# Kernel optimization log

Measured on AMD Instinct MI355X. Metric: run time of the kernel, lower is better.

Reference implementation:

```python
import jax, jax.numpy as jnp
import numpy as np

SCALE = 0.02  # init scale for weight matrices


def setup_inputs() -> dict:
    B, M, H = 2048, 64, 1024
    key = jax.random.key(0)
    ks = jax.random.split(key, 10)
    inp = {
        "pose_embed": jax.random.normal(ks[0], (B, H), jnp.float32),
        "query_embed": jax.random.normal(ks[1], (B, H), jnp.float32),
        "h": jax.random.normal(ks[2], (B, H), jnp.float32),
        "c": jax.random.normal(ks[3], (B, H), jnp.float32),
        "memory": jax.random.normal(ks[4], (B, M, H), jnp.float32),
        "W_ih": jax.random.normal(ks[5], (4 * H, H), jnp.float32) * SCALE,
        "W_hh": jax.random.normal(ks[6], (4 * H, H), jnp.float32) * SCALE,
        "b_ih": jnp.zeros((4 * H,), jnp.float32),
        "b_hh": jnp.zeros((4 * H,), jnp.float32),
        "Wq": jax.random.normal(ks[7], (H, H), jnp.float32) * SCALE,
        "bq": jnp.zeros((H,), jnp.float32),
        "Wk": jax.random.normal(ks[8], (H, H), jnp.float32) * SCALE,
        "bk": jnp.zeros((H,), jnp.float32),
        "Wv": jax.random.normal(ks[9], (H, H), jnp.float32) * SCALE,
        "bv": jnp.zeros((H,), jnp.float32),
    }
    return inp


def reference(pose_embed, query_embed, h, c, memory,
              W_ih, W_hh, b_ih, b_hh, Wq, bq, Wk, bk, Wv, bv):
    H = pose_embed.shape[-1]
    # --- LSTMCell step (torch gate order: i, f, g, o) ---
    gates = pose_embed @ W_ih.T + b_ih + h @ W_hh.T + b_hh  # [B, 4H]
    i_g, f_g, g_g, o_g = jnp.split(gates, 4, axis=-1)
    c_new = jax.nn.sigmoid(f_g) * c + jax.nn.sigmoid(i_g) * jnp.tanh(g_g)
    h_new = jax.nn.sigmoid(o_g) * jnp.tanh(c_new)
    # --- FIFO memory update (detach, pop oldest, append new h) ---
    mem = jnp.concatenate(
        [memory[:, 1:], jax.lax.stop_gradient(h_new)[:, None]], axis=1)  # [B, M, H]
    # --- single-query attention over memory ---
    Q = query_embed @ Wq.T + bq                       # [B, H]
    K = mem @ Wk.T + bk                               # [B, M, H]
    V = mem @ Wv.T + bv                               # [B, M, H]
    scores = jnp.einsum('bh,bmh->bm', Q, K) / jnp.sqrt(jnp.float32(H))
    attn = jax.nn.softmax(scores, axis=-1)            # [B, M]
    attended = jnp.einsum('bm,bmh->bh', attn, V)      # [B, H]
    return attended, h_new, c_new
```

## Files before the change

### kernel.cpp

```cpp
#include <hip/hip_runtime.h>
#include <stdint.h>

typedef __attribute__((ext_vector_type(8))) short short8;
typedef __attribute__((ext_vector_type(4))) float f32x4;
typedef unsigned short u16;

__device__ __forceinline__ u16 f2bf(float f) {
  union { float f; uint32_t u; } v; v.f = f;
  return (u16)((v.u + 0x7FFFu + ((v.u >> 16) & 1u)) >> 16);
}

__device__ __forceinline__ void gl_lds16(const void* g, void* l) {
  __builtin_amdgcn_global_load_lds(
      (const __attribute__((address_space(1))) void*)g,
      (__attribute__((address_space(3))) void*)l, 16, 0, 0);
}

__global__ __launch_bounds__(256) void gemm_bt(
    const u16* __restrict__ A, const u16* __restrict__ B,
    float* __restrict__ Cf, u16* __restrict__ Cb,
    const float* __restrict__ bias1,
    int M, int N, int K)
{
  __shared__ __align__(16) u16 As[128 * 32];
  __shared__ __align__(16) u16 Bs[128 * 32];
  const int t = threadIdx.x;
  const int lane = t & 63;
  const int w = t >> 6;
  const int wr = w >> 1, wc = w & 1;
  const int m0 = blockIdx.y * 128, n0 = blockIdx.x * 128;
  const int lr = lane & 15;
  const int lk = (lane >> 4) * 8;
  const int srow = t >> 2;
  const int scol = (t & 3) * 8;

  const u16* gA = A + (size_t)(m0 + srow) * K + scol;
  const u16* gB = B + (size_t)(n0 + srow) * K + scol;

  f32x4 acc[4][4] = {};

  for (int k0 = 0; k0 < K; k0 += 32) {
    gl_lds16(gA,                  As + t * 8);
    gl_lds16(gA + (size_t)64 * K, As + 2048 + t * 8);
    gl_lds16(gB,                  Bs + t * 8);
    gl_lds16(gB + (size_t)64 * K, Bs + 2048 + t * 8);
    gA += 32; gB += 32;
    __syncthreads();

    short8 a[4], b[4];
#pragma unroll
    for (int m = 0; m < 4; ++m)
      a[m] = *(const short8*)(As + (wr * 64 + m * 16 + lr) * 32 + lk);
#pragma unroll
    for (int n = 0; n < 4; ++n)
      b[n] = *(const short8*)(Bs + (wc * 64 + n * 16 + lr) * 32 + lk);
#pragma unroll
    for (int m = 0; m < 4; ++m)
#pragma unroll
      for (int n = 0; n < 4; ++n)
        acc[m][n] = __builtin_amdgcn_mfma_f32_16x16x32_bf16(a[m], b[n], acc[m][n], 0, 0, 0);
    __syncthreads();
  }

#pragma unroll
  for (int n = 0; n < 4; ++n) {
    int col = n0 + wc * 64 + n * 16 + lr;
    float bsum = bias1 ? bias1[col] : 0.f;
#pragma unroll
    for (int m = 0; m < 4; ++m) {
#pragma unroll
      for (int r = 0; r < 4; ++r) {
        int row = m0 + wr * 64 + m * 16 + (lane >> 4) * 4 + r;
        float vv = acc[m][n][r] + bsum;
        if (Cf) Cf[(size_t)row * N + col] = vv;
        if (Cb) Cb[(size_t)row * N + col] = f2bf(vv);
      }
    }
  }
}

__global__ __launch_bounds__(256) void prep_k(
    const float* __restrict__ pose, const float* __restrict__ h,
    const float* __restrict__ W_ih, const float* __restrict__ W_hh,
    const float* __restrict__ query, const float* __restrict__ Wv,
    const float* __restrict__ Wq, const float* __restrict__ Wk,
    u16* __restrict__ xcat, u16* __restrict__ wcat,
    u16* __restrict__ qry, u16* __restrict__ wvb,
    u16* __restrict__ wqb, u16* __restrict__ wktb)
{
  __shared__ u16 tile[64][65];
  int blk = blockIdx.x;
  int t = threadIdx.x;
  if (blk >= 16384) {
    int tblk = blk - 16384;
    int tr = (tblk >> 4) * 64, tc = (tblk & 15) * 64;
    int tx = t & 63;
    int ty = (t >> 6) * 16;
#pragma unroll
    for (int i = 0; i < 16; ++i)
      tile[ty + i][tx] = f2bf(Wk[(size_t)(tr + ty + i) * 1024 + tc + tx]);
    __syncthreads();
#pragma unroll
    for (int i = 0; i < 16; ++i)
      wktb[(size_t)(tc + ty + i) * 1024 + tr + tx] = tile[tx][ty + i];
    return;
  }
  const float* src; u16* dst; int ostride, ooff, base;
  if (blk < 2048)       { src = pose;  dst = xcat; ostride = 2048; ooff = 0;    base = 0; }
  else if (blk < 4096)  { src = h;     dst = xcat; ostride = 2048; ooff = 1024; base = 2048; }
  else if (blk < 8192)  { src = W_ih;  dst = wcat; ostride = 2048; ooff = 0;    base = 4096; }
  else if (blk < 12288) { src = W_hh;  dst = wcat; ostride = 2048; ooff = 1024; base = 8192; }
  else if (blk < 14336) { src = query; dst = qry;  ostride = 1024; ooff = 0;    base = 12288; }
  else if (blk < 15360) { src = Wv;    dst = wvb;  ostride = 1024; ooff = 0;    base = 14336; }
  else                  { src = Wq;    dst = wqb;  ostride = 1024; ooff = 0;    base = 15360; }
  int r = blk - base;
  int cc = t * 4;
  float4 v = *(const float4*)(src + (size_t)r * 1024 + cc);
  ushort4 o; o.x = f2bf(v.x); o.y = f2bf(v.y); o.z = f2bf(v.z); o.w = f2bf(v.w);
  *(ushort4*)(dst + (size_t)r * ostride + ooff + cc) = o;
}

__global__ __launch_bounds__(256, 3) void mega_k(
    const u16* __restrict__ Xcat, const u16* __restrict__ Wcat,
    float* __restrict__ gates,
    const float* __restrict__ b_ih, const float* __restrict__ b_hh,
    const float* __restrict__ Qk, const float* __restrict__ mem,
    float* __restrict__ attst)
{
  __shared__ __align__(16) u16 As[128 * 32];
  __shared__ __align__(16) u16 Bs[128 * 32];
  const int blk = blockIdx.x;
  const int t = threadIdx.x;
  const int lane = t & 63;

  if (blk % 3 != 2) {
    const int gid = (blk / 3) * 2 + (blk % 3);
    const int m0 = (gid >> 5) * 128, n0 = (gid & 31) * 128;
    const int w = t >> 6;
    const int wr = w >> 1, wc = w & 1;
    const int lr = lane & 15;
    const int lk = (lane >> 4) * 8;
    const int srow = t >> 2;
    const int scol = (t & 3) * 8;

    const u16* gA = Xcat + (size_t)(m0 + srow) * 2048 + scol;
    const u16* gB = Wcat + (size_t)(n0 + srow) * 2048 + scol;

    f32x4 acc[4][4] = {};
    for (int k0 = 0; k0 < 2048; k0 += 32) {
      gl_lds16(gA,                    As + t * 8);
      gl_lds16(gA + (size_t)64 * 2048, As + 2048 + t * 8);
      gl_lds16(gB,                    Bs + t * 8);
      gl_lds16(gB + (size_t)64 * 2048, Bs + 2048 + t * 8);
      gA += 32; gB += 32;
      __syncthreads();
      short8 a[4], b[4];
#pragma unroll
      for (int m = 0; m < 4; ++m)
        a[m] = *(const short8*)(As + (wr * 64 + m * 16 + lr) * 32 + lk);
#pragma unroll
      for (int n = 0; n < 4; ++n)
        b[n] = *(const short8*)(Bs + (wc * 64 + n * 16 + lr) * 32 + lk);
#pragma unroll
      for (int m = 0; m < 4; ++m)
#pragma unroll
        for (int n = 0; n < 4; ++n)
          acc[m][n] = __builtin_amdgcn_mfma_f32_16x16x32_bf16(a[m], b[n], acc[m][n], 0, 0, 0);
      __syncthreads();
    }
#pragma unroll
    for (int n = 0; n < 4; ++n) {
      int col = n0 + wc * 64 + n * 16 + lr;
      float bsum = b_ih[col] + b_hh[col];
#pragma unroll
      for (int m = 0; m < 4; ++m)
#pragma unroll
        for (int r = 0; r < 4; ++r) {
          int row = m0 + wr * 64 + m * 16 + (lane >> 4) * 4 + r;
          gates[(size_t)row * 4096 + col] = acc[m][n][r] + bsum;
        }
    }
  } else {
    const int ablk = blk / 3;
    const int wv_id = t >> 6;
    for (int bi = 0; bi < 2; ++bi) {
      const int b = ablk * 8 + wv_id * 2 + bi;
      const float* q = Qk + (size_t)b * 1024;
      float4 qv[4];
#pragma unroll
      for (int i = 0; i < 4; ++i)
        qv[i] = *(const float4*)(q + (i * 64 + lane) * 4);
      const float* mb = mem + (size_t)b * 65536;

      float m_run = -3e38f, l = 0.f;
      float4 cx[4] = {};

      for (int qd = 0; qd < 15; ++qd) {
        const float* r0 = mb + (size_t)(1 + qd * 4) * 1024;
        float4 rv[4][4];
        float s[4] = {0.f, 0.f, 0.f, 0.f};
#pragma unroll
        for (int rr = 0; rr < 4; ++rr)
#pragma unroll
          for (int i = 0; i < 4; ++i) {
            rv[rr][i] = *(const float4*)(r0 + rr * 1024 + (i * 64 + lane) * 4);
            s[rr] += rv[rr][i].x * qv[i].x + rv[rr][i].y * qv[i].y +
                     rv[rr][i].z * qv[i].z + rv[rr][i].w * qv[i].w;
          }
#pragma unroll
        for (int rr = 0; rr < 4; ++rr) {
#pragma unroll
          for (int off = 32; off; off >>= 1) s[rr] += __shfl_xor(s[rr], off);
          s[rr] *= 0.03125f;
        }
#pragma unroll
        for (int rr = 0; rr < 4; ++rr) {
          if (s[rr] <= m_run + 8.f) {
            float e = __expf(s[rr] - m_run);
            l += e;
#pragma unroll
            for (int i = 0; i < 4; ++i) {
              cx[i].x += e * rv[rr][i].x; cx[i].y += e * rv[rr][i].y;
              cx[i].z += e * rv[rr][i].z; cx[i].w += e * rv[rr][i].w;
            }
          } else {
            float sc = __expf(m_run - s[rr]);
            m_run = s[rr];
            l = l * sc + 1.f;
#pragma unroll
            for (int i = 0; i < 4; ++i) {
              cx[i].x = cx[i].x * sc + rv[rr][i].x; cx[i].y = cx[i].y * sc + rv[rr][i].y;
              cx[i].z = cx[i].z * sc + rv[rr][i].z; cx[i].w = cx[i].w * sc + rv[rr][i].w;
            }
          }
        }
      }
      for (int r = 61; r <= 63; ++r) {
        const float* row = mb + (size_t)r * 1024;
        float4 rv[4];
        float s = 0.f;
#pragma unroll
        for (int i = 0; i < 4; ++i) {
          rv[i] = *(const float4*)(row + (i * 64 + lane) * 4);
          s += rv[i].x * qv[i].x + rv[i].y * qv[i].y + rv[i].z * qv[i].z + rv[i].w * qv[i].w;
        }
#pragma unroll
        for (int off = 32; off; off >>= 1) s += __shfl_xor(s, off);
        s *= 0.03125f;
        if (s <= m_run + 8.f) {
          float e = __expf(s - m_run);
          l += e;
#pragma unroll
          for (int i = 0; i < 4; ++i) {
            cx[i].x += e * rv[i].x; cx[i].y += e * rv[i].y;
            cx[i].z += e * rv[i].z; cx[i].w += e * rv[i].w;
          }
        } else {
          float sc = __expf(m_run - s);
          m_run = s;
          l = l * sc + 1.f;
#pragma unroll
          for (int i = 0; i < 4; ++i) {
            cx[i].x = cx[i].x * sc + rv[i].x; cx[i].y = cx[i].y * sc + rv[i].y;
            cx[i].z = cx[i].z * sc + rv[i].z; cx[i].w = cx[i].w * sc + rv[i].w;
          }
        }
      }
      float* st = attst + (size_t)b * 1032;
#pragma unroll
      for (int i = 0; i < 4; ++i)
        *(float4*)(st + (i * 64 + lane) * 4) = cx[i];
      if (lane == 0) { st[1024] = m_run; st[1025] = l; }
    }
  }
}

__global__ __launch_bounds__(256) void lstmfin_k(
    const float* __restrict__ gates, const float* __restrict__ c,
    const float* __restrict__ Qk, const float* __restrict__ attst,
    float* __restrict__ out_h, float* __restrict__ out_c,
    u16* __restrict__ ctxb)
{
  const int b = blockIdx.x;
  const int t = threadIdx.x;
  const int lane = t & 63, wv_id = t >> 6;
  const int p = t * 4;
  const float* g = gates + (size_t)b * 4096;
  float4 ig = *(const float4*)(g + p);
  float4 fg = *(const float4*)(g + 1024 + p);
  float4 gg = *(const float4*)(g + 2048 + p);
  float4 og = *(const float4*)(g + 3072 + p);
  float4 cv = *(const float4*)(c + (size_t)b * 1024 + p);

  float hn[4], cn[4];
  {
    float igs[4] = {ig.x, ig.y, ig.z, ig.w};
    float fgs[4] = {fg.x, fg.y, fg.z, fg.w};
    float ggs[4] = {gg.x, gg.y, gg.z, gg.w};
    float ogs[4] = {og.x, og.y, og.z, og.w};
    float cvs[4] = {cv.x, cv.y, cv.z, cv.w};
#pragma unroll
    for (int j = 0; j < 4; ++j) {
      float si = 1.f / (1.f + __expf(-igs[j]));
      float sf = 1.f / (1.f + __expf(-fgs[j]));
      float so = 1.f / (1.f + __expf(-ogs[j]));
      float tg = 2.f / (1.f + __expf(-2.f * ggs[j])) - 1.f;
      cn[j] = sf * cvs[j] + si * tg;
      float tc2 = 2.f / (1.f + __expf(-2.f * cn[j])) - 1.f;
      hn[j] = so * tc2;
    }
  }
  *(float4*)(out_c + (size_t)b * 1024 + p) = make_float4(cn[0], cn[1], cn[2], cn[3]);
  *(float4*)(out_h + (size_t)b * 1024 + p) = make_float4(hn[0], hn[1], hn[2], hn[3]);

  float4 qv = *(const float4*)(Qk + (size_t)b * 1024 + p);
  float part = qv.x * hn[0] + qv.y * hn[1] + qv.z * hn[2] + qv.w * hn[3];
#pragma unroll
  for (int off = 32; off; off >>= 1) part += __shfl_xor(part, off);
  __shared__ float red[4];
  if (lane == 0) red[wv_id] = part;
  __syncthreads();
  float s_last = (red[0] + red[1] + red[2] + red[3]) * 0.03125f;

  const float* st = attst + (size_t)b * 1032;
  float m_run = st[1024], l = st[1025];
  float4 cx = *(const float4*)(st + p);
  if (s_last <= m_run + 8.f) {
    float e = __expf(s_last - m_run);
    l += e;
    cx.x += e * hn[0]; cx.y += e * hn[1]; cx.z += e * hn[2]; cx.w += e * hn[3];
  } else {
    float sc = __expf(m_run - s_last);
    l = l * sc + 1.f;
    cx.x = cx.x * sc + hn[0]; cx.y = cx.y * sc + hn[1];
    cx.z = cx.z * sc + hn[2]; cx.w = cx.w * sc + hn[3];
  }
  float inv = 1.f / l;
  ushort4 o;
  o.x = f2bf(cx.x * inv); o.y = f2bf(cx.y * inv);
  o.z = f2bf(cx.z * inv); o.w = f2bf(cx.w * inv);
  *(ushort4*)(ctxb + (size_t)b * 1024 + p) = o;
}

extern "C" void kernel_launch(void* const* d_in, const int* in_sizes, int n_in,
                              void* d_out, int out_size, void* d_ws, size_t ws_size,
                              hipStream_t stream) {
  const int Bb = 2048, Hh = 1024;
  const float* pose  = (const float*)d_in[0];
  const float* query = (const float*)d_in[1];
  const float* h     = (const float*)d_in[2];
  const float* c     = (const float*)d_in[3];
  const float* mem   = (const float*)d_in[4];
  const float* W_ih  = (const float*)d_in[5];
  const float* W_hh  = (const float*)d_in[6];
  const float* b_ih  = (const float*)d_in[7];
  const float* b_hh  = (const float*)d_in[8];
  const float* Wq    = (const float*)d_in[9];
  const float* bq    = (const float*)d_in[10];
  const float* Wk    = (const float*)d_in[11];
  const float* Wv    = (const float*)d_in[13];
  const float* bv    = (const float*)d_in[14];

  float* out_att = (float*)d_out;
  float* out_h   = out_att + (size_t)Bb * Hh;
  float* out_c   = out_h + (size_t)Bb * Hh;

  char* wp = (char*)d_ws;
  auto alloc = [&](size_t bytes) {
    char* p = wp; wp += (bytes + 255) & ~(size_t)255; return p;
  };
  u16*   Xcat  = (u16*)alloc((size_t)2048 * 2048 * 2);
  u16*   Wcat  = (u16*)alloc((size_t)4096 * 2048 * 2);
  u16*   Qryb  = (u16*)alloc((size_t)2048 * 1024 * 2);
  u16*   Wqb   = (u16*)alloc((size_t)1024 * 1024 * 2);
  u16*   WkTb  = (u16*)alloc((size_t)1024 * 1024 * 2);
  u16*   Qbf   = (u16*)alloc((size_t)2048 * 1024 * 2);
  u16*   Wvb   = (u16*)alloc((size_t)1024 * 1024 * 2);
  float* gates = (float*)alloc((size_t)2048 * 4096 * 4);
  float* Qk    = (float*)alloc((size_t)2048 * 1024 * 4);
  u16*   ctxb  = (u16*)alloc((size_t)2048 * 1024 * 2);
  float* attst = (float*)Qryb;

  prep_k<<<16640, 256, 0, stream>>>(pose, h, W_ih, W_hh, query, Wv, Wq, Wk,
                                    Xcat, Wcat, Qryb, Wvb, Wqb, WkTb);

  gemm_bt<<<dim3(8, 16), 256, 0, stream>>>(
      Qryb, Wqb, nullptr, Qbf, bq, 2048, 1024, 1024);

  gemm_bt<<<dim3(8, 16), 256, 0, stream>>>(
      Qbf, WkTb, Qk, nullptr, nullptr, 2048, 1024, 1024);

  mega_k<<<768, 256, 0, stream>>>(Xcat, Wcat, gates, b_ih, b_hh, Qk, mem, attst);

  lstmfin_k<<<2048, 256, 0, stream>>>(gates, c, Qk, attst, out_h, out_c, ctxb);

  gemm_bt<<<dim3(8, 16), 256, 0, stream>>>(
      ctxb, Wvb, out_att, nullptr, bv, 2048, 1024, 1024);
}
```

Measured before the change: 264.2 us.

## Precompute Wq·Wk product, store gates in bf16, software-pipeline attention rows

The query-key projection is reassociated: a 1024x1024 weight product G = Wk^T Wq plus a bias vector bq·Wk is computed first, then a single GEMM over the query batch replaces the two chained batch GEMMs. Gates are now written and read as bf16 instead of fp32, which halves that intermediate traffic at some cost in precision. The attention part of the fused kernel now handles two batch rows at once with double-buffered pair loads. This adds an atomic-based bias kernel and a memset launch.

```diff
diff --git a/kernel.cpp b/kernel.cpp
--- a/kernel.cpp
+++ b/kernel.cpp
@@ -8,6 +8,9 @@
 __device__ __forceinline__ u16 f2bf(float f) {
   union { float f; uint32_t u; } v; v.f = f;
   return (u16)((v.u + 0x7FFFu + ((v.u >> 16) & 1u)) >> 16);
+}
+__device__ __forceinline__ float bf2f(u16 u) {
+  union { uint32_t u; float f; } v; v.u = (uint32_t)u << 16; return v.f;
 }
 
 __device__ __forceinline__ void gl_lds16(const void* g, void* l) {
@@ -86,23 +89,25 @@
     const float* __restrict__ Wq, const float* __restrict__ Wk,
     u16* __restrict__ xcat, u16* __restrict__ wcat,
     u16* __restrict__ qry, u16* __restrict__ wvb,
-    u16* __restrict__ wqb, u16* __restrict__ wktb)
+    u16* __restrict__ wqtb, u16* __restrict__ wktb)
 {
   __shared__ u16 tile[64][65];
   int blk = blockIdx.x;
   int t = threadIdx.x;
-  if (blk >= 16384) {
-    int tblk = blk - 16384;
+  if (blk >= 15360) {
+    const float* src; u16* dst; int tblk;
+    if (blk < 15616) { src = Wq; dst = wqtb; tblk = blk - 15360; }
+    else             { src = Wk; dst = wktb; tblk = blk - 15616; }
     int tr = (tblk >> 4) * 64, tc = (tblk & 15) * 64;
     int tx = t & 63;
     int ty = (t >> 6) * 16;
 #pragma unroll
     for (int i = 0; i < 16; ++i)
-      tile[ty + i][tx] = f2bf(Wk[(size_t)(tr + ty + i) * 1024 + tc + tx]);
+      tile[ty + i][tx] = f2bf(src[(size_t)(tr + ty + i) * 1024 + tc + tx]);
     __syncthreads();
 #pragma unroll
     for (int i = 0; i < 16; ++i)
-      wktb[(size_t)(tc + ty + i) * 1024 + tr + tx] = tile[tx][ty + i];
+      dst[(size_t)(tc + ty + i) * 1024 + tr + tx] = tile[tx][ty + i];
     return;
   }
   const float* src; u16* dst; int ostride, ooff, base;
@@ -111,8 +116,7 @@
   else if (blk < 8192)  { src = W_ih;  dst = wcat; ostride = 2048; ooff = 0;    base = 4096; }
   else if (blk < 12288) { src = W_hh;  dst = wcat; ostride = 2048; ooff = 1024; base = 8192; }
   else if (blk < 14336) { src = query; dst = qry;  ostride = 1024; ooff = 0;    base = 12288; }
-  else if (blk < 15360) { src = Wv;    dst = wvb;  ostride = 1024; ooff = 0;    base = 14336; }
-  else                  { src = Wq;    dst = wqb;  ostride = 1024; ooff = 0;    base = 15360; }
+  else                  { src = Wv;    dst = wvb;  ostride = 1024; ooff = 0;    base = 14336; }
   int r = blk - base;
   int cc = t * 4;
   float4 v = *(const float4*)(src + (size_t)r * 1024 + cc);
@@ -120,9 +124,72 @@
   *(ushort4*)(dst + (size_t)r * ostride + ooff + cc) = o;
 }
 
+__global__ __launch_bounds__(256) void bqwk_k(
+    const float* __restrict__ bq, const float* __restrict__ Wk,
+    float* __restrict__ qkb)
+{
+  int n = blockIdx.x * 256 + threadIdx.x;
+  int j0 = blockIdx.y * 64;
+  float s = 0.f;
+#pragma unroll 8
+  for (int j = j0; j < j0 + 64; ++j) s += bq[j] * Wk[(size_t)j * 1024 + n];
+  atomicAdd(&qkb[n], s);
+}
+
+__device__ __forceinline__ void load_pair(const float* __restrict__ base, int lane,
+                                          float4 rv[2][4]) {
+#pragma unroll
+  for (int r = 0; r < 2; ++r)
+#pragma unroll
+    for (int i = 0; i < 4; ++i)
+      rv[r][i] = *(const float4*)(base + r * 1024 + (i * 64 + lane) * 4);
+}
+
+__device__ __forceinline__ void accum_row(const float4 rv[4], float s,
+                                          float& m_run, float& l, float4 cx[4]) {
+  if (s <= m_run + 8.f) {
+    float e = __expf(s - m_run);
+    l += e;
+#pragma unroll
+    for (int i = 0; i < 4; ++i) {
+      cx[i].x += e * rv[i].x; cx[i].y += e * rv[i].y;
+      cx[i].z += e * rv[i].z; cx[i].w += e * rv[i].w;
+    }
+  } else {
+    float sc = __expf(m_run - s);
+    m_run = s;
+    l = l * sc + 1.f;
+#pragma unroll
+    for (int i = 0; i < 4; ++i) {
+      cx[i].x = cx[i].x * sc + rv[i].x; cx[i].y = cx[i].y * sc + rv[i].y;
+      cx[i].z = cx[i].z * sc + rv[i].z; cx[i].w = cx[i].w * sc + rv[i].w;
+    }
+  }
+}
+
+__device__ __forceinline__ void compute_pair(const float4 rv[2][4], const float4 qv[4],
+                                             float& m_run, float& l, float4 cx[4]) {
+  float s0 = 0.f, s1 = 0.f;
+#pragma unroll
+  for (int i = 0; i < 4; ++i) {
+    s0 += rv[0][i].x * qv[i].x + rv[0][i].y * qv[i].y +
+          rv[0][i].z * qv[i].z + rv[0][i].w * qv[i].w;
+    s1 += rv[1][i].x * qv[i].x + rv[1][i].y * qv[i].y +
+          rv[1][i].z * qv[i].z + rv[1][i].w * qv[i].w;
+  }
+#pragma unroll
+  for (int off = 32; off; off >>= 1) {
+    s0 += __shfl_xor(s0, off);
+    s1 += __shfl_xor(s1, off);
+  }
+  s0 *= 0.03125f; s1 *= 0.03125f;
+  accum_row(rv[0], s0, m_run, l, cx);
+  accum_row(rv[1], s1, m_run, l, cx);
+}
+
 __global__ __launch_bounds__(256, 3) void mega_k(
     const u16* __restrict__ Xcat, const u16* __restrict__ Wcat,
-    float* __restrict__ gates,
+    u16* __restrict__ gates,
     const float* __restrict__ b_ih, const float* __restrict__ b_hh,
     const float* __restrict__ Qk, const float* __restrict__ mem,
     float* __restrict__ attst)
@@ -148,9 +215,9 @@
 
     f32x4 acc[4][4] = {};
     for (int k0 = 0; k0 < 2048; k0 += 32) {
-      gl_lds16(gA,                    As + t * 8);
+      gl_lds16(gA,                     As + t * 8);
       gl_lds16(gA + (size_t)64 * 2048, As + 2048 + t * 8);
-      gl_lds16(gB,                    Bs + t * 8);
+      gl_lds16(gB,                     Bs + t * 8);
       gl_lds16(gB + (size_t)64 * 2048, Bs + 2048 + t * 8);
       gA += 32; gB += 32;
       __syncthreads();
@@ -177,106 +244,77 @@
 #pragma unroll
         for (int r = 0; r < 4; ++r) {
           int row = m0 + wr * 64 + m * 16 + (lane >> 4) * 4 + r;
-          gates[(size_t)row * 4096 + col] = acc[m][n][r] + bsum;
+          gates[(size_t)row * 4096 + col] = f2bf(acc[m][n][r] + bsum);
         }
     }
   } else {
     const int ablk = blk / 3;
     const int wv_id = t >> 6;
-    for (int bi = 0; bi < 2; ++bi) {
-      const int b = ablk * 8 + wv_id * 2 + bi;
-      const float* q = Qk + (size_t)b * 1024;
-      float4 qv[4];
-#pragma unroll
-      for (int i = 0; i < 4; ++i)
-        qv[i] = *(const float4*)(q + (i * 64 + lane) * 4);
-      const float* mb = mem + (size_t)b * 65536;
-
-      float m_run = -3e38f, l = 0.f;
-      float4 cx[4] = {};
-
-      for (int qd = 0; qd < 15; ++qd) {
-        const float* r0 = mb + (size_t)(1 + qd * 4) * 1024;
-        float4 rv[4][4];
-        float s[4] = {0.f, 0.f, 0.f, 0.f};
-#pragma unroll
-        for (int rr = 0; rr < 4; ++rr)
-#pragma unroll
-          for (int i = 0; i < 4; ++i) {
-            rv[rr][i] = *(const float4*)(r0 + rr * 1024 + (i * 64 + lane) * 4);
-            s[rr] += rv[rr][i].x * qv[i].x + rv[rr][i].y * qv[i].y +
-                     rv[rr][i].z * qv[i].z + rv[rr][i].w * qv[i].w;
-          }
-#pragma unroll
-        for (int rr = 0; rr < 4; ++rr) {
-#pragma unroll
-          for (int off = 32; off; off >>= 1) s[rr] += __shfl_xor(s[rr], off);
-          s[rr] *= 0.03125f;
-        }
-#pragma unroll
-        for (int rr = 0; rr < 4; ++rr) {
-          if (s[rr] <= m_run + 8.f) {
-            float e = __expf(s[rr] - m_run);
-            l += e;
-#pragma unroll
-            for (int i = 0; i < 4; ++i) {
-              cx[i].x += e * rv[rr][i].x; cx[i].y += e * rv[rr][i].y;
-              cx[i].z += e * rv[rr][i].z; cx[i].w += e * rv[rr][i].w;
-            }
-          } else {
-            float sc = __expf(m_run - s[rr]);
-            m_run = s[rr];
-            l = l * sc + 1.f;
-#pragma unroll
-            for (int i = 0; i < 4; ++i) {
-              cx[i].x = cx[i].x * sc + rv[rr][i].x; cx[i].y = cx[i].y * sc + rv[rr][i].y;
-              cx[i].z = cx[i].z * sc + rv[rr][i].z; cx[i].w = cx[i].w * sc + rv[rr][i].w;
-            }
-          }
-        }
+    const int b0 = ablk * 8 + wv_id * 2;
+    const int b1 = b0 + 1;
+
+    float4 qv0[4], qv1[4];
+#pragma unroll
+    for (int i = 0; i < 4; ++i) {
+      qv0[i] = *(const float4*)(Qk + (size_t)b0 * 1024 + (i * 64 + lane) * 4);
+      qv1[i] = *(const float4*)(Qk + (size_t)b1 * 1024 + (i * 64 + lane) * 4);
+    }
+    const float* mb0 = mem + (size_t)b0 * 65536;
+    const float* mb1 = mem + (size_t)b1 * 65536;
+
+    float m0r = -3e38f, l0 = 0.f, m1r = -3e38f, l1 = 0.f;
+    float4 cx0[4] = {}, cx1[4] = {};
+    float4 rv0[2][4], rv1[2][4];
+
+    load_pair(mb0 + 1024, lane, rv0);
+    load_pair(mb1 + 1024, lane, rv1);
+
+    for (int p = 0; p < 31; ++p) {
+      compute_pair(rv0, qv0, m0r, l0, cx0);
+      if (p < 30) load_pair(mb0 + (size_t)(3 + 2 * p) * 1024, lane, rv0);
+      compute_pair(rv1, qv1, m1r, l1, cx1);
+      if (p < 30) load_pair(mb1 + (size_t)(3 + 2 * p) * 1024, lane, rv1);
+    }
+    {
+      float4 rs0[4], rs1[4];
+#pragma unroll
+      for (int i = 0; i < 4; ++i) {
+        rs0[i] = *(const float4*)(mb0 + 63 * 1024 + (i * 64 + lane) * 4);
+        rs1[i] = *(const float4*)(mb1 + 63 * 1024 + (i * 64 + lane) * 4);
       }
-      for (int r = 61; r <= 63; ++r) {
-        const float* row = mb + (size_t)r * 1024;
-        float4 rv[4];
-        float s = 0.f;
-#pragma unroll
-        for (int i = 0; i < 4; ++i) {
-          rv[i] = *(const float4*)(row + (i * 64 + lane) * 4);
-          s += rv[i].x * qv[i].x + rv[i].y * qv[i].y + rv[i].z * qv[i].z + rv[i].w * qv[i].w;
-        }
-#pragma unroll
-        for (int off = 32; off; off >>= 1) s += __shfl_xor(s, off);
-        s *= 0.03125f;
-        if (s <= m_run + 8.f) {
-          float e = __expf(s - m_run);
-          l += e;
-#pragma unroll
-          for (int i = 0; i < 4; ++i) {
-            cx[i].x += e * rv[i].x; cx[i].y += e * rv[i].y;
-            cx[i].z += e * rv[i].z; cx[i].w += e * rv[i].w;
-          }
-        } else {
-          float sc = __expf(m_run - s);
-          m_run = s;
-          l = l * sc + 1.f;
-#pragma unroll
-          for (int i = 0; i < 4; ++i) {
-            cx[i].x = cx[i].x * sc + rv[i].x; cx[i].y = cx[i].y * sc + rv[i].y;
-            cx[i].z = cx[i].z * sc + rv[i].z; cx[i].w = cx[i].w * sc + rv[i].w;
-          }
-        }
+      float s0 = 0.f, s1 = 0.f;
+#pragma unroll
+      for (int i = 0; i < 4; ++i) {
+        s0 += rs0[i].x * qv0[i].x + rs0[i].y * qv0[i].y +
+              rs0[i].z * qv0[i].z + rs0[i].w * qv0[i].w;
+        s1 += rs1[i].x * qv1[i].x + rs1[i].y * qv1[i].y +
+              rs1[i].z * qv1[i].z + rs1[i].w * qv1[i].w;
       }
-      float* st = attst + (size_t)b * 1032;
-#pragma unroll
-      for (int i = 0; i < 4; ++i)
-        *(float4*)(st + (i * 64 + lane) * 4) = cx[i];
-      if (lane == 0) { st[1024] = m_run; st[1025] = l; }
+#pragma unroll
+      for (int off = 32; off; off >>= 1) {
+        s0 += __shfl_xor(s0, off);
+        s1 += __shfl_xor(s1, off);
+      }
+      s0 *= 0.03125f; s1 *= 0.03125f;
+      accum_row(rs0, s0, m0r, l0, cx0);
+      accum_row(rs1, s1, m1r, l1, cx1);
+    }
+    float* st0 = attst + (size_t)b0 * 1032;
+    float* st1 = attst + (size_t)b1 * 1032;
+#pragma unroll
+    for (int i = 0; i < 4; ++i) {
+      *(float4*)(st0 + (i * 64 + lane) * 4) = cx0[i];
+      *(float4*)(st1 + (i * 64 + lane) * 4) = cx1[i];
+    }
+    if (lane == 0) {
+      st0[1024] = m0r; st0[1025] = l0;
+      st1[1024] = m1r; st1[1025] = l1;
     }
   }
 }
 
 __global__ __launch_bounds__(256) void lstmfin_k(
-    const float* __restrict__ gates, const float* __restrict__ c,
+    const u16* __restrict__ gates, const float* __restrict__ c,
     const float* __restrict__ Qk, const float* __restrict__ attst,
     float* __restrict__ out_h, float* __restrict__ out_c,
     u16* __restrict__ ctxb)
@@ -285,19 +323,19 @@
   const int t = threadIdx.x;
   const int lane = t & 63, wv_id = t >> 6;
   const int p = t * 4;
-  const float* g = gates + (size_t)b * 4096;
-  float4 ig = *(const float4*)(g + p);
-  float4 fg = *(const float4*)(g + 1024 + p);
-  float4 gg = *(const float4*)(g + 2048 + p);
-  float4 og = *(const float4*)(g + 3072 + p);
+  const u16* g = gates + (size_t)b * 4096;
+  ushort4 igu = *(const ushort4*)(g + p);
+  ushort4 fgu = *(const ushort4*)(g + 1024 + p);
+  ushort4 ggu = *(const ushort4*)(g + 2048 + p);
+  ushort4 ogu = *(const ushort4*)(g + 3072 + p);
   float4 cv = *(const float4*)(c + (size_t)b * 1024 + p);
 
   float hn[4], cn[4];
   {
-    float igs[4] = {ig.x, ig.y, ig.z, ig.w};
-    float fgs[4] = {fg.x, fg.y, fg.z, fg.w};
-    float ggs[4] = {gg.x, gg.y, gg.z, gg.w};
-    float ogs[4] = {og.x, og.y, og.z, og.w};
+    float igs[4] = {bf2f(igu.x), bf2f(igu.y), bf2f(igu.z), bf2f(igu.w)};
+    float fgs[4] = {bf2f(fgu.x), bf2f(fgu.y), bf2f(fgu.z), bf2f(fgu.w)};
+    float ggs[4] = {bf2f(ggu.x), bf2f(ggu.y), bf2f(ggu.z), bf2f(ggu.w)};
+    float ogs[4] = {bf2f(ogu.x), bf2f(ogu.y), bf2f(ogu.z), bf2f(ogu.w)};
     float cvs[4] = {cv.x, cv.y, cv.z, cv.w};
 #pragma unroll
     for (int j = 0; j < 4; ++j) {
@@ -372,23 +410,27 @@
   u16*   Xcat  = (u16*)alloc((size_t)2048 * 2048 * 2);
   u16*   Wcat  = (u16*)alloc((size_t)4096 * 2048 * 2);
   u16*   Qryb  = (u16*)alloc((size_t)2048 * 1024 * 2);
-  u16*   Wqb   = (u16*)alloc((size_t)1024 * 1024 * 2);
+  u16*   WqTb  = (u16*)alloc((size_t)1024 * 1024 * 2);
   u16*   WkTb  = (u16*)alloc((size_t)1024 * 1024 * 2);
-  u16*   Qbf   = (u16*)alloc((size_t)2048 * 1024 * 2);
+  u16*   Gb    = (u16*)alloc((size_t)1024 * 1024 * 2);
   u16*   Wvb   = (u16*)alloc((size_t)1024 * 1024 * 2);
-  float* gates = (float*)alloc((size_t)2048 * 4096 * 4);
+  u16*   gates = (u16*)alloc((size_t)2048 * 4096 * 2);
+  float* qkb   = (float*)alloc((size_t)1024 * 4);
   float* Qk    = (float*)alloc((size_t)2048 * 1024 * 4);
   u16*   ctxb  = (u16*)alloc((size_t)2048 * 1024 * 2);
   float* attst = (float*)Qryb;
 
-  prep_k<<<16640, 256, 0, stream>>>(pose, h, W_ih, W_hh, query, Wv, Wq, Wk,
-                                    Xcat, Wcat, Qryb, Wvb, Wqb, WkTb);
+  prep_k<<<15872, 256, 0, stream>>>(pose, h, W_ih, W_hh, query, Wv, Wq, Wk,
+                                    Xcat, Wcat, Qryb, Wvb, WqTb, WkTb);
+
+  hipMemsetAsync(qkb, 0, 1024 * sizeof(float), stream);
+  bqwk_k<<<dim3(4, 16), 256, 0, stream>>>(bq, Wk, qkb);
+
+  gemm_bt<<<dim3(8, 8), 256, 0, stream>>>(
+      WkTb, WqTb, nullptr, Gb, nullptr, 1024, 1024, 1024);
 
   gemm_bt<<<dim3(8, 16), 256, 0, stream>>>(
-      Qryb, Wqb, nullptr, Qbf, bq, 2048, 1024, 1024);
-
-  gemm_bt<<<dim3(8, 16), 256, 0, stream>>>(
-      Qbf, WkTb, Qk, nullptr, nullptr, 2048, 1024, 1024);
+      Qryb, Gb, Qk, nullptr, qkb, 2048, 1024, 1024);
 
   mega_k<<<768, 256, 0, stream>>>(Xcat, Wcat, gates, b_ih, b_hh, Qk, mem, attst);
 
```

New measurement: 286.4 us. 8.4% more time.
